# Kernel optimization log

Hardware: AMD Instinct MI355X
Metric: run time of the kernel (lower is better)

Reference implementation:

```python
import jax, jax.numpy as jnp
import numpy as np

B, H, W, C_IN, C_HID = 32, 64, 64, 384, 128

def setup_inputs() -> dict:
    key = jax.random.key(0)
    k0, k1, k2 = jax.random.split(key, 3)
    dino_features = jax.random.normal(k0, (B, H, W, C_IN), dtype=jnp.float32)
    # Xavier-uniform(gain=0.5) bounds for conv weights, HWIO layout
    fan1 = C_IN * 9 + C_HID * 9
    lim1 = 0.5 * np.sqrt(6.0 / fan1)
    W1 = jax.random.uniform(k1, (3, 3, C_IN, C_HID), minval=-lim1, maxval=lim1, dtype=jnp.float32)
    b1 = jnp.zeros((C_HID,), dtype=jnp.float32)
    fan2 = C_HID + 1
    lim2 = 0.5 * np.sqrt(6.0 / fan2)
    W2 = jax.random.uniform(k2, (1, 1, C_HID, 1), minval=-lim2, maxval=lim2, dtype=jnp.float32)
    b2 = jnp.zeros((1,), dtype=jnp.float32)
    return {"dino_features": dino_features, "W1": W1, "b1": b1, "W2": W2, "b2": b2}

def _conv(x, w, pad):
    # x: NHWC, w: HWIO -> NHWC
    return jax.lax.conv_general_dilated(
        x, w, window_strides=(1, 1), padding=pad,
        dimension_numbers=("NHWC", "HWIO", "NHWC"))

def reference(dino_features, W1, b1, W2, b2):
    # conv3x3 (pad 1) -> ReLU -> conv1x1 -> sigmoid; output (B,H,W,1)
    h = jax.nn.relu(_conv(dino_features, W1, ((1, 1), (1, 1))) + b1)
    logits = _conv(h, W2, ((0, 0), (0, 0))) + b2
    return jax.nn.sigmoid(logits)
```

## Files before the change

kernel.cpp:

```cpp
#include <hip/hip_runtime.h>
#include <hip/hip_bf16.h>
#include <math.h>


typedef __attribute__((ext_vector_type(8))) unsigned short ushort8;
typedef __attribute__((ext_vector_type(8))) __bf16 bf16x8;
typedef __attribute__((ext_vector_type(4))) float floatx4;

#define HPX 324
#define BUFE 10368

static __device__ __forceinline__ unsigned short f2bf_rne(float f) {
  union { float f; unsigned int u; } x; x.f = f;
  unsigned int u = x.u;
  return (unsigned short)((u + 0x7fffu + ((u >> 16) & 1u)) >> 16);
}

static __device__ __forceinline__ ushort8 pack8(const float* v) {
  ushort8 r;
#pragma unroll
  for (int i = 0; i < 4; ++i) {
    __hip_bfloat162 p = __float22bfloat162_rn(make_float2(v[2 * i], v[2 * i + 1]));
    union { __hip_bfloat162 b; unsigned int u; } c;
    c.b = p;
    r[2 * i] = (unsigned short)(c.u & 0xffffu);
    r[2 * i + 1] = (unsigned short)(c.u >> 16);
  }
  return r;
}

__global__ void prep_w1_kernel(const float* __restrict__ W1,
                               unsigned short* __restrict__ W1b) {
  __shared__ unsigned short tile[32 * 128];
  const int kk = blockIdx.x;
  const int o = kk / 12;
  const int chunk = kk - o * 12;
  const float* src = W1 + (o * 384 + chunk * 32) * 128;
  const int t = threadIdx.x;
#pragma unroll
  for (int i = 0; i < 16; ++i) {
    int idx = t + i * 256;
    int c = idx >> 7;
    int n = idx & 127;
    tile[n * 32 + c] = f2bf_rne(src[idx]);
  }
  __syncthreads();
  unsigned short* dst = W1b + kk * 4096;
#pragma unroll
  for (int i = 0; i < 16; ++i) {
    int idx = t + i * 256;
    dst[idx] = tile[idx];
  }
}

#define SLOADP(DST, JJ, CHOFF)                                               \
  {                                                                          \
    float tf[8];                                                             \
    if ((smask >> (JJ)) & 1) {                                               \
      *(float4*)&tf[0] = *(const float4*)(x + soff[JJ] + (CHOFF));           \
      *(float4*)&tf[4] = *(const float4*)(x + soff[JJ] + (CHOFF) + 4);       \
    } else {                                                                 \
      _Pragma("unroll") for (int e = 0; e < 8; ++e) tf[e] = 0.0f;            \
    }                                                                        \
    DST = pack8(tf);                                                         \
  }

#define SWRITE8(SRC, JJ, WB)                                                 \
  if ((JJ) < 2 || t < 272)                                                   \
    *(ushort8*)&Ah[(WB) + ((t + ((JJ) << 9)) << 3)] = SRC;

__global__ __launch_bounds__(512, 4) void conv_fused_kernel(
    const float* __restrict__ x, const unsigned short* __restrict__ W1b,
    const float* __restrict__ b1, const float* __restrict__ W2,
    const float* __restrict__ b2, float* __restrict__ out) {
  __shared__ alignas(16) unsigned short Ah[2 * BUFE];
  __shared__ float hsum[256 * 4];

  const int t = threadIdx.x;
  const int w = t >> 6;
  const int wm = w >> 2;
  const int wn = w & 3;
  const int lane = t & 63;
  const int g = lane >> 4;
  const int lr = lane & 15;

  const int img = blockIdx.x >> 4;
  const int tileId = blockIdx.x & 15;
  const int ty0 = (tileId >> 2) << 4;
  const int tx0 = (tileId & 3) << 4;

  int smask = 0;
  int soff[3];
#pragma unroll
  for (int j = 0; j < 3; ++j) {
    int item = t + (j << 9);
    int px = item >> 2, sub = item & 3;
    int hy = (px * 57) >> 10;
    int hx = px - hy * 18;
    int iy = ty0 + hy - 1, ix = tx0 + hx - 1;
    int v = (item < 1296) && ((unsigned)iy < 64u) && ((unsigned)ix < 64u);
    smask |= (v << j);
    int iyc = v ? iy : 0, ixc = v ? ix : 0;
    soff[j] = ((((img << 6) + iyc) << 6) + ixc) * 384 + sub * 8;
  }

  const int boff = ((wn * 32 + lr) << 5) + (g << 3);
  const int aoffl = (lr << 5) + (g << 3);

  floatx4 acc[8][2] = {};

  ushort8 su0, su1, su2;

  {
    SLOADP(su0, 0, 0)
    SLOADP(su1, 1, 0)
    SLOADP(su2, 2, 0)
    SWRITE8(su0, 0, 0)
    SWRITE8(su1, 1, 0)
    SWRITE8(su2, 2, 0)
  }
  __syncthreads();

  for (int c = 0; c < 12; ++c) {
    const int rb = (c & 1) * BUFE;
    const int wb = BUFE - rb;
    const int choff = (c + 1) << 5;
    const bool pf = (c < 11);

#pragma unroll
    for (int ox = 0; ox < 3; ++ox) {
      bf16x8 bf[3][2];
#pragma unroll
      for (int oy = 0; oy < 3; ++oy) {
        const unsigned short* bp =
            W1b + (((oy * 3 + ox) * 12 + c) << 12) + boff;
        bf[oy][0] = *(const bf16x8*)bp;
        bf[oy][1] = *(const bf16x8*)(bp + 512);
      }

      if (pf) {
        if (ox == 0) {
          SLOADP(su0, 0, choff)
        } else if (ox == 1) {
          SWRITE8(su0, 0, wb)
          SLOADP(su1, 1, choff)
        } else {
          SWRITE8(su1, 1, wb)
          SLOADP(su2, 2, choff)
        }
      }

      __builtin_amdgcn_s_setprio(1);
#pragma unroll
      for (int hl = 0; hl < 10; ++hl) {
        const int hg = wm * 8 + hl;
        const bf16x8 af =
            *(const bf16x8*)&Ah[rb + ((hg * 18 + ox) << 5) + aoffl];
#pragma unroll
        for (int oy = 0; oy < 3; ++oy) {
          const int mi = hl - oy;
          if (mi >= 0 && mi < 8) {
            acc[mi][0] = __builtin_amdgcn_mfma_f32_16x16x32_bf16(
                af, bf[oy][0], acc[mi][0], 0, 0, 0);
            acc[mi][1] = __builtin_amdgcn_mfma_f32_16x16x32_bf16(
                af, bf[oy][1], acc[mi][1], 0, 0, 0);
          }
        }
      }
      __builtin_amdgcn_s_setprio(0);
    }
    if (pf) { SWRITE8(su2, 2, wb) }
    __syncthreads();
  }

  const float b1v0 = b1[wn * 32 + lr];
  const float b1v1 = b1[wn * 32 + 16 + lr];
  const float w2v0 = W2[wn * 32 + lr];
  const float w2v1 = W2[wn * 32 + 16 + lr];
#pragma unroll
  for (int mi = 0; mi < 8; ++mi) {
#pragma unroll
    for (int r = 0; r < 4; ++r) {
      float h0 = fmaxf(acc[mi][0][r] + b1v0, 0.0f);
      float h1 = fmaxf(acc[mi][1][r] + b1v1, 0.0f);
      float v = h0 * w2v0 + h1 * w2v1;
      v += __shfl_xor(v, 1);
      v += __shfl_xor(v, 2);
      v += __shfl_xor(v, 4);
      v += __shfl_xor(v, 8);
      if (lr == 0) {
        int m = (wm * 8 + mi) * 16 + g * 4 + r;
        hsum[m * 4 + wn] = v;
      }
    }
  }
  __syncthreads();
  if (t < 256) {
    float4 p = *(const float4*)&hsum[t * 4];
    float s = p.x + p.y + p.z + p.w + b2[0];
    float sig = 1.0f / (1.0f + expf(-s));
    int prow = t >> 4, pcol = t & 15;
    out[((((img << 6) + ty0 + prow) << 6) + tx0 + pcol)] = sig;
  }
}

extern "C" void kernel_launch(void* const* d_in, const int* in_sizes, int n_in,
                              void* d_out, int out_size, void* d_ws, size_t ws_size,
                              hipStream_t stream) {
  const float* x  = (const float*)d_in[0];
  const float* W1 = (const float*)d_in[1];
  const float* b1 = (const float*)d_in[2];
  const float* W2 = (const float*)d_in[3];
  const float* b2 = (const float*)d_in[4];
  float* out = (float*)d_out;
  unsigned short* W1b = (unsigned short*)d_ws;

  prep_w1_kernel<<<108, 256, 0, stream>>>(W1, W1b);
  conv_fused_kernel<<<512, 512, 0, stream>>>(x, W1b, b1, W2, b2, out);
}
```

Measured before the change: 333.2 us.

## Switch conv to 32x32x16 MFMA with 8x32 tiles and swizzled LDS layout

Replaces the 16x16x32 bf16 MFMA with the 32x32x16 variant and changes the spatial tile from 16x16 to 8 rows by 32 columns, so each MFMA covers one 32-pixel row against 32 output channels. The LDS halo buffer grows to a 10x34 layout and gets an XOR-style chunk swizzle on writes and reads to avoid bank conflicts. The input staging now keeps fp32 registers and packs to bf16 at write time. The aim is fewer MFMA issues and fewer A-fragment loads per FLOP, at the cost of a larger halo (more redundant loads) and a longer epilogue reduction.

```diff
diff --git a/kernel.cpp b/kernel.cpp
--- a/kernel.cpp
+++ b/kernel.cpp
@@ -5,10 +5,10 @@
 
 typedef __attribute__((ext_vector_type(8))) unsigned short ushort8;
 typedef __attribute__((ext_vector_type(8))) __bf16 bf16x8;
-typedef __attribute__((ext_vector_type(4))) float floatx4;
-
-#define HPX 324
-#define BUFE 10368
+typedef __attribute__((ext_vector_type(16))) float floatx16;
+
+#define HW2 34
+#define BUF 10880
 
 static __device__ __forceinline__ unsigned short f2bf_rne(float f) {
   union { float f; unsigned int u; } x; x.f = f;
@@ -53,144 +53,141 @@
   }
 }
 
-#define SLOADP(DST, JJ, CHOFF)                                               \
-  {                                                                          \
-    float tf[8];                                                             \
-    if ((smask >> (JJ)) & 1) {                                               \
-      *(float4*)&tf[0] = *(const float4*)(x + soff[JJ] + (CHOFF));           \
-      *(float4*)&tf[4] = *(const float4*)(x + soff[JJ] + (CHOFF) + 4);       \
-    } else {                                                                 \
-      _Pragma("unroll") for (int e = 0; e < 8; ++e) tf[e] = 0.0f;            \
-    }                                                                        \
-    DST = pack8(tf);                                                         \
-  }
-
-#define SWRITE8(SRC, JJ, WB)                                                 \
-  if ((JJ) < 2 || t < 272)                                                   \
-    *(ushort8*)&Ah[(WB) + ((t + ((JJ) << 9)) << 3)] = SRC;
+#define SLOADF(DST, JJ, CHOFF)                                               \
+  if ((smask >> (JJ)) & 1) {                                                 \
+    *(float4*)&DST[0] = *(const float4*)(x + soff[JJ] + (CHOFF));            \
+    *(float4*)&DST[4] = *(const float4*)(x + soff[JJ] + (CHOFF) + 4);        \
+  } else {                                                                   \
+    _Pragma("unroll") for (int e = 0; e < 8; ++e) DST[e] = 0.0f;             \
+  }
+
+#define SWR(SRC, JJ, WB)                                                     \
+  if ((JJ) < 2 || t < 336)                                                   \
+    *(ushort8*)&Ah[(WB) + (witem[JJ] << 3)] = pack8(SRC);
 
 __global__ __launch_bounds__(512, 4) void conv_fused_kernel(
     const float* __restrict__ x, const unsigned short* __restrict__ W1b,
     const float* __restrict__ b1, const float* __restrict__ W2,
     const float* __restrict__ b2, float* __restrict__ out) {
-  __shared__ alignas(16) unsigned short Ah[2 * BUFE];
+  __shared__ alignas(16) unsigned short Ah[2 * BUF];
   __shared__ float hsum[256 * 4];
 
   const int t = threadIdx.x;
   const int w = t >> 6;
-  const int wm = w >> 2;
+  const int wm4 = (w >> 2) << 2;
   const int wn = w & 3;
   const int lane = t & 63;
-  const int g = lane >> 4;
-  const int lr = lane & 15;
+  const int l5 = lane >> 5;
+  const int lq = lane & 31;
 
   const int img = blockIdx.x >> 4;
-  const int tileId = blockIdx.x & 15;
-  const int ty0 = (tileId >> 2) << 4;
-  const int tx0 = (tileId & 3) << 4;
+  const int tid = blockIdx.x & 15;
+  const int ty0 = (tid >> 1) << 3;
+  const int tx0 = (tid & 1) << 5;
 
   int smask = 0;
-  int soff[3];
+  int soff[3], witem[3];
 #pragma unroll
   for (int j = 0; j < 3; ++j) {
     int item = t + (j << 9);
     int px = item >> 2, sub = item & 3;
-    int hy = (px * 57) >> 10;
-    int hx = px - hy * 18;
+    int hy = px / 34;
+    int hx = px - hy * 34;
     int iy = ty0 + hy - 1, ix = tx0 + hx - 1;
-    int v = (item < 1296) && ((unsigned)iy < 64u) && ((unsigned)ix < 64u);
+    int v = (item < 1360) && ((unsigned)iy < 64u) && ((unsigned)ix < 64u);
     smask |= (v << j);
     int iyc = v ? iy : 0, ixc = v ? ix : 0;
     soff[j] = ((((img << 6) + iyc) << 6) + ixc) * 384 + sub * 8;
-  }
-
-  const int boff = ((wn * 32 + lr) << 5) + (g << 3);
-  const int aoffl = (lr << 5) + (g << 3);
-
-  floatx4 acc[8][2] = {};
-
-  ushort8 su0, su1, su2;
+    witem[j] = (px << 2) | ((sub + hy + (hx & 3)) & 3);
+  }
+
+  const int bofflane = ((wn * 32 + lq) << 5) + (l5 << 3);
+  const int aL = lq << 5;
+
+  floatx16 acc[4] = {};
+
+  float sA[8], sB[8];
 
   {
-    SLOADP(su0, 0, 0)
-    SLOADP(su1, 1, 0)
-    SLOADP(su2, 2, 0)
-    SWRITE8(su0, 0, 0)
-    SWRITE8(su1, 1, 0)
-    SWRITE8(su2, 2, 0)
+    SLOADF(sA, 0, 0)
+    SLOADF(sB, 1, 0)
+    SWR(sA, 0, 0)
+    SLOADF(sA, 2, 0)
+    SWR(sB, 1, 0)
+    SWR(sA, 2, 0)
   }
   __syncthreads();
 
   for (int c = 0; c < 12; ++c) {
-    const int rb = (c & 1) * BUFE;
-    const int wb = BUFE - rb;
+    const int rb = (c & 1) * BUF;
+    const int wbuf = BUF - rb;
     const int choff = (c + 1) << 5;
     const bool pf = (c < 11);
 
 #pragma unroll
     for (int ox = 0; ox < 3; ++ox) {
-      bf16x8 bf[3][2];
-#pragma unroll
-      for (int oy = 0; oy < 3; ++oy) {
-        const unsigned short* bp =
-            W1b + (((oy * 3 + ox) * 12 + c) << 12) + boff;
-        bf[oy][0] = *(const bf16x8*)bp;
-        bf[oy][1] = *(const bf16x8*)(bp + 512);
-      }
-
-      if (pf) {
-        if (ox == 0) {
-          SLOADP(su0, 0, choff)
-        } else if (ox == 1) {
-          SWRITE8(su0, 0, wb)
-          SLOADP(su1, 1, choff)
-        } else {
-          SWRITE8(su1, 1, wb)
-          SLOADP(su2, 2, choff)
+      const int vmx = l5 + ((ox + lq) & 3);
+#pragma unroll
+      for (int ks = 0; ks < 2; ++ks) {
+        const int p = ox * 2 + ks;
+
+        bf16x8 bf[3];
+#pragma unroll
+        for (int oy = 0; oy < 3; ++oy) {
+          bf[oy] = *(const bf16x8*)(W1b + (((oy * 3 + ox) * 12 + c) << 12) +
+                                    bofflane + (ks << 4));
         }
-      }
-
-      __builtin_amdgcn_s_setprio(1);
-#pragma unroll
-      for (int hl = 0; hl < 10; ++hl) {
-        const int hg = wm * 8 + hl;
-        const bf16x8 af =
-            *(const bf16x8*)&Ah[rb + ((hg * 18 + ox) << 5) + aoffl];
-#pragma unroll
-        for (int oy = 0; oy < 3; ++oy) {
-          const int mi = hl - oy;
-          if (mi >= 0 && mi < 8) {
-            acc[mi][0] = __builtin_amdgcn_mfma_f32_16x16x32_bf16(
-                af, bf[oy][0], acc[mi][0], 0, 0, 0);
-            acc[mi][1] = __builtin_amdgcn_mfma_f32_16x16x32_bf16(
-                af, bf[oy][1], acc[mi][1], 0, 0, 0);
+
+        if (pf) {
+          if (p == 0) {
+            SLOADF(sA, 0, choff)
+          } else if (p == 2) {
+            SWR(sA, 0, wbuf)
+            SLOADF(sB, 1, choff)
+          } else if (p == 4) {
+            SWR(sB, 1, wbuf)
+            SLOADF(sA, 2, choff)
           }
         }
+
+        __builtin_amdgcn_s_setprio(1);
+#pragma unroll
+        for (int hl = 0; hl < 6; ++hl) {
+          const int gp = (hl + 2 * ks + vmx) & 3;
+          const bf16x8 af = *(const bf16x8*)&Ah[rb +
+              (((wm4 + hl) * 34 + ox) << 5) + aL + (gp << 3)];
+#pragma unroll
+          for (int oy = 0; oy < 3; ++oy) {
+            const int mt = hl - oy;
+            if (mt >= 0 && mt < 4) {
+              acc[mt] = __builtin_amdgcn_mfma_f32_32x32x16_bf16(
+                  af, bf[oy], acc[mt], 0, 0, 0);
+            }
+          }
+        }
+        __builtin_amdgcn_s_setprio(0);
       }
-      __builtin_amdgcn_s_setprio(0);
     }
-    if (pf) { SWRITE8(su2, 2, wb) }
+    if (pf) { SWR(sA, 2, wbuf) }
     __syncthreads();
   }
 
-  const float b1v0 = b1[wn * 32 + lr];
-  const float b1v1 = b1[wn * 32 + 16 + lr];
-  const float w2v0 = W2[wn * 32 + lr];
-  const float w2v1 = W2[wn * 32 + 16 + lr];
-#pragma unroll
-  for (int mi = 0; mi < 8; ++mi) {
-#pragma unroll
-    for (int r = 0; r < 4; ++r) {
-      float h0 = fmaxf(acc[mi][0][r] + b1v0, 0.0f);
-      float h1 = fmaxf(acc[mi][1][r] + b1v1, 0.0f);
-      float v = h0 * w2v0 + h1 * w2v1;
+  const float b1v = b1[wn * 32 + lq];
+  const float w2v = W2[wn * 32 + lq];
+#pragma unroll
+  for (int mt = 0; mt < 4; ++mt) {
+#pragma unroll
+    for (int r = 0; r < 16; ++r) {
+      float v = fmaxf(acc[mt][r] + b1v, 0.0f) * w2v;
       v += __shfl_xor(v, 1);
       v += __shfl_xor(v, 2);
       v += __shfl_xor(v, 4);
       v += __shfl_xor(v, 8);
-      if (lr == 0) {
-        int m = (wm * 8 + mi) * 16 + g * 4 + r;
-        hsum[m * 4 + wn] = v;
+      v += __shfl_xor(v, 16);
+      if (lq == 0) {
+        int pxx = (r & 3) + ((r >> 2) << 3) + (l5 << 2);
+        int row = wm4 + mt;
+        hsum[((row << 5) + pxx) * 4 + wn] = v;
       }
     }
   }
@@ -199,8 +196,8 @@
     float4 p = *(const float4*)&hsum[t * 4];
     float s = p.x + p.y + p.z + p.w + b2[0];
     float sig = 1.0f / (1.0f + expf(-s));
-    int prow = t >> 4, pcol = t & 15;
-    out[((((img << 6) + ty0 + prow) << 6) + tx0 + pcol)] = sig;
+    int row = t >> 5, col = t & 31;
+    out[(((img << 6) + ty0 + row) << 6) + tx0 + col] = sig;
   }
 }
 
```

Result: slower. 365.6 us (+9.7%).
